# Kernel tuning notes

Hardware: AMD Instinct MI355X
Metric: run time of the kernel (lower is better)

## Reference

```python
import math
import jax, jax.numpy as jnp
import numpy as np

B, N, D, H = 2, 2048, 1024, 16

def setup_inputs() -> dict:
    key = jax.random.key(0)
    ks = jax.random.split(key, 5)
    x = jax.random.normal(ks[0], (B, N, D), dtype=jnp.float32)
    # causal mask: True = masked (matches masked_fill semantics)
    mask = jnp.broadcast_to(jnp.triu(jnp.ones((N, N), dtype=bool), k=1), (B, N, N))
    sc = 0.02
    Wqkv = jax.random.normal(ks[1], (3 * D, D), dtype=jnp.float32) * sc
    bqkv = jax.random.normal(ks[2], (3 * D,), dtype=jnp.float32) * sc
    Wo = jax.random.normal(ks[3], (D, D), dtype=jnp.float32) * sc
    bo = jax.random.normal(ks[4], (D,), dtype=jnp.float32) * sc
    return {"x": x, "mask": mask, "Wqkv": Wqkv, "bqkv": bqkv, "Wo": Wo, "bo": bo}

def reference(x, mask, Wqkv, bqkv, Wo, bo):
    b, n, d = x.shape
    h = H
    s = d // h
    qkv = x @ Wqkv.T + bqkv                       # [b, n, 3d]
    q, k, v = jnp.split(qkv, 3, axis=2)           # each [b, n, d]
    def heads(z):
        return z.reshape(b, n, h, s).transpose(0, 2, 1, 3)  # [b, h, n, s]
    q, k, v = heads(q), heads(k), heads(v)
    q = q / jnp.asarray(math.sqrt(s), q.dtype)
    a = jnp.einsum('bhqs,bhks->bhqk', q, k)       # [b, h, n, n]
    a = jnp.where(mask[:, None, :, :], -jnp.inf, a)
    a = jax.nn.softmax(a, axis=-1)
    y = jnp.einsum('bhqk,bhks->bhqs', a, v)       # [b, h, n, s]
    y = y.transpose(0, 2, 1, 3).reshape(b, n, d)
    return y @ Wo.T + bo
```

## Files before the change

kernel.cpp:

```cpp
#include <hip/hip_runtime.h>
#include <hip/hip_bf16.h>
#include <stdint.h>

#define BB 2
#define NN 2048
#define DD 1024
#define HH 16
#define SS 64

typedef short short8 __attribute__((ext_vector_type(8)));
typedef float f32x4 __attribute__((ext_vector_type(4)));

__device__ __forceinline__ float bf2f(uint16_t u) {
    return __uint_as_float(((uint32_t)u) << 16);
}
__device__ __forceinline__ uint16_t f2bf(float f) {
    uint32_t u = __float_as_uint(f);
    return (uint16_t)((u + 0x7FFFu + ((u >> 16) & 1u)) >> 16);
}
__device__ __forceinline__ short8 cvt8(float4 a, float4 b) {
    short8 s;
    s[0] = (short)f2bf(a.x); s[1] = (short)f2bf(a.y);
    s[2] = (short)f2bf(a.z); s[3] = (short)f2bf(a.w);
    s[4] = (short)f2bf(b.x); s[5] = (short)f2bf(b.y);
    s[6] = (short)f2bf(b.z); s[7] = (short)f2bf(b.w);
    return s;
}

__device__ __forceinline__ void load_lds16(const uint16_t* g, uint16_t* l) {
    __builtin_amdgcn_global_load_lds(
        (const __attribute__((address_space(1))) void*)g,
        (__attribute__((address_space(3))) void*)l, 16, 0, 0);
}

#define XE  (4096 * 1024)
#define WQE (3072 * 1024)
#define WOE (1024 * 1024)

__global__ __launch_bounds__(256) void cvt_all(
    const float* __restrict__ x, const float* __restrict__ wq,
    const float* __restrict__ wo, uint16_t* __restrict__ dst)
{
    int i = (blockIdx.x * 256 + threadIdx.x) * 8;
    const float* src;
    int off;
    if (i < XE)            { src = x;  off = i; }
    else if (i < XE + WQE) { src = wq; off = i - XE; }
    else                   { src = wo; off = i - XE - WQE; }
    float4 a = *(const float4*)(src + off);
    float4 b = *(const float4*)(src + off + 4);
    *(short8*)(dst + i) = cvt8(a, b);
}

__global__ __launch_bounds__(256) void gemm_qkv(
    const uint16_t* __restrict__ X, const uint16_t* __restrict__ W,
    const float* __restrict__ bias,
    uint16_t* __restrict__ Qb, uint16_t* __restrict__ Kb, uint16_t* __restrict__ Vt)
{
    __shared__ __align__(16) uint16_t smem[18432];
    uint16_t* As = smem;
    uint16_t* Bs = smem + 4096;

    const int tid = threadIdx.x;
    const int w = tid >> 6, l = tid & 63;
    const int lq = l & 15, lg = l >> 4;
    const int wm = w >> 1, wn = w & 1;
    const int m0 = blockIdx.y * 128;
    const int n0 = blockIdx.x * 128;

    f32x4 acc[4][4] = {};

    for (int k0 = 0; k0 < 1024; k0 += 32) {
        __syncthreads();
        #pragma unroll
        for (int j = 0; j < 2; ++j) {
            const int c = (j * 4 + w) * 64 + l;
            load_lds16(X + (size_t)(m0 + (c >> 2)) * 1024 + k0 + (c & 3) * 8,
                       As + (j * 4 + w) * 512);
            load_lds16(W + (size_t)(n0 + (c >> 2)) * 1024 + k0 + (c & 3) * 8,
                       Bs + (j * 4 + w) * 512);
        }
        __syncthreads();
        short8 af[4], bfr[4];
        #pragma unroll
        for (int mi = 0; mi < 4; ++mi)
            af[mi] = *(const short8*)&As[(wm * 64 + mi * 16 + lq) * 32 + lg * 8];
        #pragma unroll
        for (int ni = 0; ni < 4; ++ni)
            bfr[ni] = *(const short8*)&Bs[(wn * 64 + ni * 16 + lq) * 32 + lg * 8];
        #pragma unroll
        for (int mi = 0; mi < 4; ++mi)
            #pragma unroll
            for (int ni = 0; ni < 4; ++ni)
                acc[mi][ni] = __builtin_amdgcn_mfma_f32_16x16x32_bf16(
                    af[mi], bfr[ni], acc[mi][ni], 0, 0, 0);
    }

    __syncthreads();
    const int part = n0 >> 10;
    const int hh = ((n0 + wn * 64) & 1023) >> 6;
    const int mrow0 = m0 + wm * 64;
    const int bh = (mrow0 >> 11) * 16 + hh;
    const int tok0 = mrow0 & 2047;
    const float scl = (part == 0) ? 0.125f * 1.44269504089f : 1.0f;

    float bias4[4];
    #pragma unroll
    for (int ni = 0; ni < 4; ++ni)
        bias4[ni] = bias[n0 + wn * 64 + ni * 16 + lq];

    uint16_t* T = smem + w * 4608;
    if (part < 2) {
        #pragma unroll
        for (int mi = 0; mi < 4; ++mi)
            #pragma unroll
            for (int ni = 0; ni < 4; ++ni)
                #pragma unroll
                for (int r = 0; r < 4; ++r)
                    T[(mi * 16 + lg * 4 + r) * 72 + ni * 16 + lq] =
                        f2bf((acc[mi][ni][r] + bias4[ni]) * scl);
    } else {
        #pragma unroll
        for (int mi = 0; mi < 4; ++mi)
            #pragma unroll
            for (int ni = 0; ni < 4; ++ni)
                #pragma unroll
                for (int r = 0; r < 4; ++r)
                    T[(ni * 16 + lq) * 72 + mi * 16 + lg * 4 + r] =
                        f2bf(acc[mi][ni][r] + bias4[ni]);
    }

    const int a0 = l >> 3, b8 = (l & 7) * 8;
    #pragma unroll
    for (int i = 0; i < 8; ++i) {
        int a = i * 8 + a0;
        short8 u = *(short8*)&T[a * 72 + b8];
        uint16_t* p;
        if (part < 2) {
            uint16_t* dst = (part == 0) ? Qb : Kb;
            p = dst + ((size_t)bh * 2048 + tok0 + a) * 64 + b8;
        } else {
            p = Vt + ((size_t)bh * 64 + a) * 2048 + tok0 + b8;
        }
        *(short8*)p = u;
    }
}

__device__ __forceinline__ void loadKf(const uint16_t* Kb, int kv0, int lq, int lg,
                                       short8 (&d)[8]) {
    #pragma unroll
    for (int n = 0; n < 4; ++n) {
        const uint16_t* kb = Kb + (size_t)(kv0 + n * 16 + lq) * 64 + lg * 8;
        d[2 * n]     = *(const short8*)kb;
        d[2 * n + 1] = *(const short8*)(kb + 32);
    }
}
__device__ __forceinline__ void loadVf(const uint16_t* Vb, int kv0, int lq, int lg,
                                       short8 (&d)[8]) {
    #pragma unroll
    for (int n = 0; n < 4; ++n) {
        const uint16_t* vb = Vb + (size_t)(n * 16 + lq) * 2048 + kv0 + lg * 8;
        d[2 * n]     = *(const short8*)vb;
        d[2 * n + 1] = *(const short8*)(vb + 32);
    }
}

#define DEFER_THR 11.5f

__global__ __launch_bounds__(128) void attn_mfma(
    const uint16_t* __restrict__ Q, const uint16_t* __restrict__ K,
    const uint16_t* __restrict__ Vt, uint16_t* __restrict__ Y)
{
    const int id = blockIdx.x;
    const int bh = id & 31;
    const int blk = 63 - (id >> 5);
    const int qt = blk >> 1;
    const int q0 = blk * 32;

    const int wv = threadIdx.x >> 6;
    const int lane = threadIdx.x & 63;
    const int lq = lane & 15;
    const int lg = lane >> 4;

    __shared__ __align__(16) uint16_t Pl[2][2][16][72];
    __shared__ float  My[32][68];
    __shared__ float2 Mml[32];

    const uint16_t* Kb = K + (size_t)bh * (2048 * 64);
    const uint16_t* Vb = Vt + (size_t)bh * (64 * 2048);
    const int b = bh >> 4, h = bh & 15;

    short8 qf[2][2];
    #pragma unroll
    for (int sub = 0; sub < 2; ++sub) {
        const uint16_t* qb = Q + ((size_t)bh * 2048 + q0 + sub * 16 + lq) * 64 + lg * 8;
        qf[sub][0] = *(const short8*)qb;
        qf[sub][1] = *(const short8*)(qb + 32);
    }

    f32x4 y[2][4] = {};
    float m[2]    = {-INFINITY, -INFINITY};
    float lsum[2] = {0.f, 0.f};

    short8 kf[8], vv[8];
    loadKf(Kb, wv * 64, lq, lg, kf);

    for (int kt = wv; kt <= qt; kt += 2) {
        const int kv0 = kt * 64;
        loadVf(Vb, kv0, lq, lg, vv);

        f32x4 z[2][4];
        __builtin_amdgcn_s_setprio(1);
        #pragma unroll
        for (int sub = 0; sub < 2; ++sub)
            #pragma unroll
            for (int n = 0; n < 4; ++n) {
                f32x4 t = {};
                t = __builtin_amdgcn_mfma_f32_16x16x32_bf16(kf[2 * n], qf[sub][0], t, 0, 0, 0);
                z[sub][n] = __builtin_amdgcn_mfma_f32_16x16x32_bf16(kf[2 * n + 1], qf[sub][1], t, 0, 0, 0);
            }
        __builtin_amdgcn_s_setprio(0);

        if (kt + 2 <= qt) loadKf(Kb, kv0 + 128, lq, lg, kf);

        #pragma unroll
        for (int sub = 0; sub < 2; ++sub) {
            if (kt == qt) {
                const int qrow = q0 + sub * 16 + lq;
                #pragma unroll
                for (int n = 0; n < 4; ++n) {
                    const int kvb = kv0 + n * 16 + lg * 4;
                    #pragma unroll
                    for (int r = 0; r < 4; ++r)
                        if (kvb + r > qrow) z[sub][n][r] = -INFINITY;
                }
            }
            float mt = -INFINITY;
            #pragma unroll
            for (int n = 0; n < 4; ++n)
                #pragma unroll
                for (int r = 0; r < 4; ++r)
                    mt = fmaxf(mt, z[sub][n][r]);
            const bool skip = __all(mt - m[sub] <= DEFER_THR);

            if (!skip) {
                float mf = fmaxf(mt, __shfl_xor(mt, 16));
                mf = fmaxf(mf, __shfl_xor(mf, 32));
                const float mn = fmaxf(m[sub], mf);
                const float sc = exp2f(m[sub] - mn);
                m[sub] = mn;
                lsum[sub] *= sc;
                float scy[4];
                #pragma unroll
                for (int r = 0; r < 4; ++r) scy[r] = __shfl(sc, lg * 4 + r);
                #pragma unroll
                for (int n = 0; n < 4; ++n)
                    #pragma unroll
                    for (int r = 0; r < 4; ++r)
                        y[sub][n][r] *= scy[r];
            }

            float ps = 0.f;
            uint32_t pk0[4], pk1[4];
            #pragma unroll
            for (int n = 0; n < 4; ++n) {
                float e0 = exp2f(z[sub][n][0] - m[sub]);
                float e1 = exp2f(z[sub][n][1] - m[sub]);
                float e2 = exp2f(z[sub][n][2] - m[sub]);
                float e3 = exp2f(z[sub][n][3] - m[sub]);
                ps += (e0 + e1) + (e2 + e3);
                asm("v_cvt_pk_bf16_f32 %0, %1, %2" : "=v"(pk0[n]) : "v"(e0), "v"(e1));
                asm("v_cvt_pk_bf16_f32 %0, %1, %2" : "=v"(pk1[n]) : "v"(e2), "v"(e3));
            }
            lsum[sub] += ps;
            #pragma unroll
            for (int n = 0; n < 4; ++n) {
                uint2 u; u.x = pk0[n]; u.y = pk1[n];
                *(uint2*)&Pl[wv][sub][lq][n * 16 + lg * 4] = u;
            }

            short8 pa0 = *(short8*)&Pl[wv][sub][lq][lg * 8];
            short8 pa1 = *(short8*)&Pl[wv][sub][lq][lg * 8 + 32];
            __builtin_amdgcn_s_setprio(1);
            #pragma unroll
            for (int n = 0; n < 4; ++n) {
                y[sub][n] = __builtin_amdgcn_mfma_f32_16x16x32_bf16(pa0, vv[2 * n], y[sub][n], 0, 0, 0);
                y[sub][n] = __builtin_amdgcn_mfma_f32_16x16x32_bf16(pa1, vv[2 * n + 1], y[sub][n], 0, 0, 0);
            }
            __builtin_amdgcn_s_setprio(0);
        }
    }

    float ls[2];
    #pragma unroll
    for (int sub = 0; sub < 2; ++sub) {
        float t = lsum[sub];
        t += __shfl_xor(t, 16);
        t += __shfl_xor(t, 32);
        ls[sub] = t;
    }

    if (wv == 1) {
        #pragma unroll
        for (int sub = 0; sub < 2; ++sub) {
            #pragma unroll
            for (int n = 0; n < 4; ++n)
                #pragma unroll
                for (int r = 0; r < 4; ++r)
                    My[sub * 16 + lg * 4 + r][n * 16 + lq] = y[sub][n][r];
            if (lg == 0) Mml[sub * 16 + lq] = make_float2(m[sub], ls[sub]);
        }
    }
    __syncthreads();
    if (wv == 0) {
        #pragma unroll
        for (int sub = 0; sub < 2; ++sub) {
            float2 o = Mml[sub * 16 + lq];
            const float m1 = o.x, l1 = o.y;
            const float mx = fmaxf(m[sub], m1);
            const float w0 = exp2f(m[sub] - mx);
            const float w1 = exp2f(m1 - mx);
            const float inv = 1.0f / (ls[sub] * w0 + l1 * w1);
            const float f0 = w0 * inv, f1 = w1 * inv;
            float f0r[4], f1r[4];
            #pragma unroll
            for (int r = 0; r < 4; ++r) {
                f0r[r] = __shfl(f0, lg * 4 + r);
                f1r[r] = __shfl(f1, lg * 4 + r);
            }
            #pragma unroll
            for (int r = 0; r < 4; ++r) {
                int token = b * 2048 + q0 + sub * 16 + lg * 4 + r;
                uint16_t* yrow = Y + (size_t)token * 1024 + h * 64;
                #pragma unroll
                for (int n = 0; n < 4; ++n) {
                    float val = y[sub][n][r] * f0r[r] +
                                My[sub * 16 + lg * 4 + r][n * 16 + lq] * f1r[r];
                    yrow[n * 16 + lq] = f2bf(val);
                }
            }
        }
    }
}

__global__ __launch_bounds__(256) void gemm_proj(
    const uint16_t* __restrict__ Yin, const uint16_t* __restrict__ W,
    const float* __restrict__ bias, float* __restrict__ out)
{
    __shared__ __align__(16) uint16_t smem[8192];
    uint16_t* As = smem;
    uint16_t* Bs = smem + 4096;

    const int tid = threadIdx.x;
    const int w = tid >> 6, l = tid & 63;
    const int lq = l & 15, lg = l >> 4;
    const int wm = w >> 1, wn = w & 1;
    const int m0 = blockIdx.y * 128;
    const int n0 = blockIdx.x * 128;

    f32x4 acc[4][4] = {};

    for (int k0 = 0; k0 < 1024; k0 += 32) {
        __syncthreads();
        #pragma unroll
        for (int j = 0; j < 2; ++j) {
            const int c = (j * 4 + w) * 64 + l;
            load_lds16(Yin + (size_t)(m0 + (c >> 2)) * 1024 + k0 + (c & 3) * 8,
                       As + (j * 4 + w) * 512);
            load_lds16(W + (size_t)(n0 + (c >> 2)) * 1024 + k0 + (c & 3) * 8,
                       Bs + (j * 4 + w) * 512);
        }
        __syncthreads();
        short8 af[4], bfr[4];
        #pragma unroll
        for (int mi = 0; mi < 4; ++mi)
            af[mi] = *(const short8*)&As[(wm * 64 + mi * 16 + lq) * 32 + lg * 8];
        #pragma unroll
        for (int ni = 0; ni < 4; ++ni)
            bfr[ni] = *(const short8*)&Bs[(wn * 64 + ni * 16 + lq) * 32 + lg * 8];
        #pragma unroll
        for (int mi = 0; mi < 4; ++mi)
            #pragma unroll
            for (int ni = 0; ni < 4; ++ni)
                acc[mi][ni] = __builtin_amdgcn_mfma_f32_16x16x32_bf16(
                    af[mi], bfr[ni], acc[mi][ni], 0, 0, 0);
    }

    const int mrow0 = m0 + wm * 64;
    const int ncol0 = n0 + wn * 64;
    float bias4[4];
    #pragma unroll
    for (int ni = 0; ni < 4; ++ni)
        bias4[ni] = bias[ncol0 + ni * 16 + lq];

    #pragma unroll
    for (int mi = 0; mi < 4; ++mi)
        #pragma unroll
        for (int r = 0; r < 4; ++r) {
            const size_t rowoff = (size_t)(mrow0 + mi * 16 + lg * 4 + r) * 1024;
            #pragma unroll
            for (int ni = 0; ni < 4; ++ni)
                out[rowoff + ncol0 + ni * 16 + lq] = acc[mi][ni][r] + bias4[ni];
        }
}


extern "C" void kernel_launch(void* const* d_in, const int* in_sizes, int n_in,
                              void* d_out, int out_size, void* d_ws, size_t ws_size,
                              hipStream_t stream) {
    const float* x    = (const float*)d_in[0];
    const float* Wqkv = (const float*)d_in[2];
    const float* bqkv = (const float*)d_in[3];
    const float* Wo   = (const float*)d_in[4];
    const float* bo   = (const float*)d_in[5];

    const size_t QK = (size_t)BB * HH * NN * SS;

    uint16_t* Xb  = (uint16_t*)d_ws;
    uint16_t* Wqb = Xb + XE;
    uint16_t* Wob = Wqb + WQE;
    uint16_t* Qb  = Wob + WOE;
    uint16_t* Kb  = Qb + QK;
    uint16_t* Vt  = Kb + QK;
    uint16_t* Yb  = Vt + QK;

    cvt_all<<<(XE + WQE + WOE) / 8 / 256, 256, 0, stream>>>(x, Wqkv, Wo, Xb);
    gemm_qkv<<<dim3(24, 32), 256, 0, stream>>>(Xb, Wqb, bqkv, Qb, Kb, Vt);
    attn_mfma<<<2048, 128, 0, stream>>>(Qb, Kb, Vt, Yb);
    gemm_proj<<<dim3(8, 32), 256, 0, stream>>>(Yb, Wob, bo, (float*)d_out);
}
```

Baseline: 149.9 us.

## Double K-step per barrier in QKV/proj GEMMs and remap blocks for XCD locality

Both GEMM kernels now load a 64-wide K slice per iteration into two LDS halves, halving the number of barrier pairs and global load issue rounds per tile. Block indices are remapped so consecutive blocks on the same XCD share weight column tiles, aiming for better L2 reuse. The projection GEMM doubles its LDS footprint, which may lower occupancy.

```diff
diff --git a/kernel.cpp b/kernel.cpp
--- a/kernel.cpp
+++ b/kernel.cpp
@@ -58,36 +58,55 @@
     uint16_t* __restrict__ Qb, uint16_t* __restrict__ Kb, uint16_t* __restrict__ Vt)
 {
     __shared__ __align__(16) uint16_t smem[18432];
-    uint16_t* As = smem;
-    uint16_t* Bs = smem + 4096;
+    uint16_t* As0 = smem;
+    uint16_t* As1 = smem + 4096;
+    uint16_t* Bs0 = smem + 8192;
+    uint16_t* Bs1 = smem + 12288;
 
     const int tid = threadIdx.x;
     const int w = tid >> 6, l = tid & 63;
     const int lq = l & 15, lg = l >> 4;
     const int wm = w >> 1, wn = w & 1;
-    const int m0 = blockIdx.y * 128;
-    const int n0 = blockIdx.x * 128;
+
+    const int flat = blockIdx.x + blockIdx.y * 24;
+    const int xcd = flat & 7, g = flat >> 3;
+    const int n0 = (xcd * 3 + (g % 3)) * 128;
+    const int m0 = (g / 3) * 128;
 
     f32x4 acc[4][4] = {};
 
-    for (int k0 = 0; k0 < 1024; k0 += 32) {
+    for (int k0 = 0; k0 < 1024; k0 += 64) {
         __syncthreads();
         #pragma unroll
         for (int j = 0; j < 2; ++j) {
             const int c = (j * 4 + w) * 64 + l;
-            load_lds16(X + (size_t)(m0 + (c >> 2)) * 1024 + k0 + (c & 3) * 8,
-                       As + (j * 4 + w) * 512);
-            load_lds16(W + (size_t)(n0 + (c >> 2)) * 1024 + k0 + (c & 3) * 8,
-                       Bs + (j * 4 + w) * 512);
+            const size_t ra = (size_t)(m0 + (c >> 2)) * 1024 + k0 + (c & 3) * 8;
+            const size_t rb = (size_t)(n0 + (c >> 2)) * 1024 + k0 + (c & 3) * 8;
+            load_lds16(X + ra,      As0 + (j * 4 + w) * 512);
+            load_lds16(X + ra + 32, As1 + (j * 4 + w) * 512);
+            load_lds16(W + rb,      Bs0 + (j * 4 + w) * 512);
+            load_lds16(W + rb + 32, Bs1 + (j * 4 + w) * 512);
         }
         __syncthreads();
         short8 af[4], bfr[4];
         #pragma unroll
         for (int mi = 0; mi < 4; ++mi)
-            af[mi] = *(const short8*)&As[(wm * 64 + mi * 16 + lq) * 32 + lg * 8];
+            af[mi] = *(const short8*)&As0[(wm * 64 + mi * 16 + lq) * 32 + lg * 8];
         #pragma unroll
         for (int ni = 0; ni < 4; ++ni)
-            bfr[ni] = *(const short8*)&Bs[(wn * 64 + ni * 16 + lq) * 32 + lg * 8];
+            bfr[ni] = *(const short8*)&Bs0[(wn * 64 + ni * 16 + lq) * 32 + lg * 8];
+        #pragma unroll
+        for (int mi = 0; mi < 4; ++mi)
+            #pragma unroll
+            for (int ni = 0; ni < 4; ++ni)
+                acc[mi][ni] = __builtin_amdgcn_mfma_f32_16x16x32_bf16(
+                    af[mi], bfr[ni], acc[mi][ni], 0, 0, 0);
+        #pragma unroll
+        for (int mi = 0; mi < 4; ++mi)
+            af[mi] = *(const short8*)&As1[(wm * 64 + mi * 16 + lq) * 32 + lg * 8];
+        #pragma unroll
+        for (int ni = 0; ni < 4; ++ni)
+            bfr[ni] = *(const short8*)&Bs1[(wn * 64 + ni * 16 + lq) * 32 + lg * 8];
         #pragma unroll
         for (int mi = 0; mi < 4; ++mi)
             #pragma unroll
@@ -347,37 +366,55 @@
     const uint16_t* __restrict__ Yin, const uint16_t* __restrict__ W,
     const float* __restrict__ bias, float* __restrict__ out)
 {
-    __shared__ __align__(16) uint16_t smem[8192];
-    uint16_t* As = smem;
-    uint16_t* Bs = smem + 4096;
+    __shared__ __align__(16) uint16_t smem[16384];
+    uint16_t* As0 = smem;
+    uint16_t* As1 = smem + 4096;
+    uint16_t* Bs0 = smem + 8192;
+    uint16_t* Bs1 = smem + 12288;
 
     const int tid = threadIdx.x;
     const int w = tid >> 6, l = tid & 63;
     const int lq = l & 15, lg = l >> 4;
     const int wm = w >> 1, wn = w & 1;
-    const int m0 = blockIdx.y * 128;
-    const int n0 = blockIdx.x * 128;
+
+    const int flat = blockIdx.x + blockIdx.y * 8;
+    const int n0 = (flat & 7) * 128;
+    const int m0 = (flat >> 3) * 128;
 
     f32x4 acc[4][4] = {};
 
-    for (int k0 = 0; k0 < 1024; k0 += 32) {
+    for (int k0 = 0; k0 < 1024; k0 += 64) {
         __syncthreads();
         #pragma unroll
         for (int j = 0; j < 2; ++j) {
             const int c = (j * 4 + w) * 64 + l;
-            load_lds16(Yin + (size_t)(m0 + (c >> 2)) * 1024 + k0 + (c & 3) * 8,
-                       As + (j * 4 + w) * 512);
-            load_lds16(W + (size_t)(n0 + (c >> 2)) * 1024 + k0 + (c & 3) * 8,
-                       Bs + (j * 4 + w) * 512);
+            const size_t ra = (size_t)(m0 + (c >> 2)) * 1024 + k0 + (c & 3) * 8;
+            const size_t rb = (size_t)(n0 + (c >> 2)) * 1024 + k0 + (c & 3) * 8;
+            load_lds16(Yin + ra,      As0 + (j * 4 + w) * 512);
+            load_lds16(Yin + ra + 32, As1 + (j * 4 + w) * 512);
+            load_lds16(W + rb,        Bs0 + (j * 4 + w) * 512);
+            load_lds16(W + rb + 32,   Bs1 + (j * 4 + w) * 512);
         }
         __syncthreads();
         short8 af[4], bfr[4];
         #pragma unroll
         for (int mi = 0; mi < 4; ++mi)
-            af[mi] = *(const short8*)&As[(wm * 64 + mi * 16 + lq) * 32 + lg * 8];
+            af[mi] = *(const short8*)&As0[(wm * 64 + mi * 16 + lq) * 32 + lg * 8];
         #pragma unroll
         for (int ni = 0; ni < 4; ++ni)
-            bfr[ni] = *(const short8*)&Bs[(wn * 64 + ni * 16 + lq) * 32 + lg * 8];
+            bfr[ni] = *(const short8*)&Bs0[(wn * 64 + ni * 16 + lq) * 32 + lg * 8];
+        #pragma unroll
+        for (int mi = 0; mi < 4; ++mi)
+            #pragma unroll
+            for (int ni = 0; ni < 4; ++ni)
+                acc[mi][ni] = __builtin_amdgcn_mfma_f32_16x16x32_bf16(
+                    af[mi], bfr[ni], acc[mi][ni], 0, 0, 0);
+        #pragma unroll
+        for (int mi = 0; mi < 4; ++mi)
+            af[mi] = *(const short8*)&As1[(wm * 64 + mi * 16 + lq) * 32 + lg * 8];
+        #pragma unroll
+        for (int ni = 0; ni < 4; ++ni)
+            bfr[ni] = *(const short8*)&Bs1[(wn * 64 + ni * 16 + lq) * 32 + lg * 8];
         #pragma unroll
         for (int mi = 0; mi < 4; ++mi)
             #pragma unroll
```

After: 141.4 us. 1.06x faster.
